# Performance work log

Hardware: AMD Instinct MI355X
Metric: run time of the kernel (lower is better)

Reference implementation:

```python
import jax, jax.numpy as jnp
import numpy as np

T, N, H = 512, 256, 256
HR, WC = 64, 128   # mdp rows (== n_actions), mdp cols
V = 64             # size of 'values' observation


def setup_inputs() -> dict:
    key = jax.random.key(0)
    ks = jax.random.split(key, 20)
    def p(i, shape):
        return (jax.random.normal(ks[i], shape, jnp.float32) / np.sqrt(shape[0])).astype(jnp.float32)
    z = lambda *s: jnp.zeros(s, jnp.float32)
    return dict(
        values=jax.random.normal(ks[0], (T, N, V), jnp.float32),
        mdp=jax.random.normal(ks[1], (N, HR, WC), jnp.float32),
        actions=jax.random.randint(ks[2], (T, N), 0, HR),
        a0=jax.random.randint(ks[3], (N,), 0, HR),
        h0=jax.random.normal(ks[4], (N, H), jnp.float32) * 0.1,
        emb_W=p(5, (WC, H)), emb_b=z(H),
        gfw_Wih=p(6, (H, 3 * H)), gfw_Whh=p(7, (H, 3 * H)), gfw_bih=z(3 * H), gfw_bhh=z(3 * H),
        gbw_Wih=p(8, (H, 3 * H)), gbw_Whh=p(9, (H, 3 * H)), gbw_bih=z(3 * H), gbw_bhh=z(3 * H),
        f0_W=p(10, (V + H, H)), f0_b=z(H),
        f1_W=p(11, (H, H)), f1_b=z(H),
        cell_Wih=p(12, (H, 3 * H)), cell_Whh=p(13, (H, 3 * H)), cell_bih=z(3 * H), cell_bhh=z(3 * H),
        critic_W=p(14, (H, 1)), critic_b=z(1),
        qg_W=p(15, (H, 2 * H)), qg_b=z(2 * H),
    )


def gru_step(x, h, Wih, Whh, bih, bhh):
    # torch GRU gate math: gates ordered (reset, update, new)
    gi = x @ Wih + bih
    gh = h @ Whh + bhh
    ir, iz, in_ = jnp.split(gi, 3, axis=-1)
    hr, hz, hn = jnp.split(gh, 3, axis=-1)
    r = jax.nn.sigmoid(ir + hr)
    z = jax.nn.sigmoid(iz + hz)
    n = jnp.tanh(in_ + r * hn)
    return (1.0 - z) * n + z * h


def run_gru(seq, Wih, Whh, bih, bhh):
    # seq: (S, N, H) -> outputs (S, N, H), zero initial state (torch default)
    h0g = jnp.zeros((seq.shape[1], Whh.shape[0]), seq.dtype)
    def step(h, x):
        hn = gru_step(x, h, Wih, Whh, bih, bhh)
        return hn, hn
    _, out = jax.lax.scan(step, h0g, seq)
    return out


def _forward(values, mdp, actions, a0, h0,
             emb_W, emb_b,
             gfw_Wih, gfw_Whh, gfw_bih, gfw_bhh,
             gbw_Wih, gbw_Whh, gbw_bih, gbw_bhh,
             f0_W, f0_b, f1_W, f1_b,
             cell_Wih, cell_Whh, cell_bih, cell_bhh,
             critic_W, critic_b, qg_W, qg_b):
    M = mdp @ emb_W + emb_b                      # (N, HR, H) line embeddings
    seq = jnp.swapaxes(M, 0, 1)                  # (HR, N, H) seq-first
    Kf = run_gru(seq, gfw_Wih, gfw_Whh, gfw_bih, gfw_bhh)
    Kb = run_gru(seq[::-1], gbw_Wih, gbw_Whh, gbw_bih, gbw_bhh)[::-1]
    K = jnp.swapaxes(jnp.concatenate([Kf, Kb], -1), 0, 1)   # (N, HR, 2H)

    a_prev = jnp.concatenate([a0[None], actions[:-1]], axis=0)  # A[t-1], t=0 wraps to hx.a
    batch = jnp.arange(M.shape[0])

    def step(h, xs):
        v_t, ap, ac = xs
        r = M[batch, ap]                         # one-hot(a_prev) @ M == row gather, (N, H)
        x = jnp.concatenate([v_t, r], axis=-1)
        x = jax.nn.relu(x @ f0_W + f0_b)
        x = jax.nn.relu(x @ f1_W + f1_b)
        h = gru_step(x, h, cell_Wih, cell_Whh, cell_bih, cell_bhh)
        k = h @ qg_W + qg_b                      # (N, 2H) query
        logits = jnp.einsum('nsd,nd->ns', K, k)  # (N, HR)
        probs = jax.nn.softmax(logits, axis=-1)
        v = h @ critic_W + critic_b              # (N, 1)
        return h, (ac.astype(jnp.float32)[:, None], v, h, probs)

    _, (a_out, v_out, h_out, p_out) = jax.lax.scan(step, h0, (values, a_prev, actions))
    # pack() order: RecurrentState fields 'a v h a_probs'
    hx = jnp.concatenate([a_out, v_out, h_out, p_out], axis=-1)  # (T, N, 2+H+HR)
    return hx


def reference(values, mdp, actions, a0, h0,
              emb_W, emb_b,
              gfw_Wih, gfw_Whh, gfw_bih, gfw_bhh,
              gbw_Wih, gbw_Whh, gbw_bih, gbw_bhh,
              f0_W, f0_b, f1_W, f1_b,
              cell_Wih, cell_Whh, cell_bih, cell_bhh,
              critic_W, critic_b, qg_W, qg_b):
    return _forward(values, mdp, actions, a0, h0,
                    emb_W, emb_b,
                    gfw_Wih, gfw_Whh, gfw_bih, gfw_bhh,
                    gbw_Wih, gbw_Whh, gbw_bih, gbw_bhh,
                    f0_W, f0_b, f1_W, f1_b,
                    cell_Wih, cell_Whh, cell_bih, cell_bhh,
                    critic_W, critic_b, qg_W, qg_b)
```

## Files before the change

kernel.cpp:

```cpp
#include <hip/hip_runtime.h>

#define TSTEPS 512
#define NBATCH 256
#define HID    256
#define TCHUNK 64
#define NCHUNK 8

typedef __attribute__((ext_vector_type(8))) short bf16x8;
typedef __attribute__((ext_vector_type(4))) float f32x4;

__device__ __forceinline__ unsigned short f2b(float x) {
    union { float f; unsigned int u; } c; c.f = x;
    unsigned int u = c.u;
    return (unsigned short)((u + 0x7fffu + ((u >> 16) & 1u)) >> 16);
}

__device__ __forceinline__ void gload_lds16(const float* g, float* l) {
    __builtin_amdgcn_global_load_lds(
        (const __attribute__((address_space(1))) unsigned int*)g,
        (__attribute__((address_space(3))) unsigned int*)l,
        16, 0, 0);
}

__device__ __forceinline__ int swzi(int row, int g) {
    return ((g ^ ((row >> 3) & 3)) << 3);
}

template<bool TRANS_B, int ACT>
__global__ __launch_bounds__(256) void gemm_f32(
    const float* __restrict__ A, long lda, long sA,
    const float* __restrict__ B, long ldb, long sB,
    const float* __restrict__ bias,
    float* __restrict__ C, long ldc, long sC,
    int M, int N, int K)
{
    __shared__ __align__(16) unsigned short As[64][32];
    __shared__ __align__(16) unsigned short Bs[64][32];
    const int z = blockIdx.z;
    A += (long)z * sA; B += (long)z * sB; C += (long)z * sC;
    const int n0 = blockIdx.x * 64, m0 = blockIdx.y * 64;
    const int tid  = threadIdx.x;
    const int lane = tid & 63, w = tid >> 6;
    const int wr = (w >> 1) * 32, wc = (w & 1) * 32;

    f32x4 acc[2][2];
#pragma unroll
    for (int i = 0; i < 2; i++)
#pragma unroll
        for (int j = 0; j < 2; j++) acc[i][j] = (f32x4){0.f, 0.f, 0.f, 0.f};

    for (int k0 = 0; k0 < K; k0 += 32) {
        {
            const int r = tid >> 2, ck = (tid & 3) << 3;
            const float* s = A + (long)(m0 + r) * lda + k0 + ck;
            float4 v0 = *(const float4*)s, v1 = *(const float4*)(s + 4);
            unsigned short* d = &As[r][swzi(r, ck >> 3)];
            d[0] = f2b(v0.x); d[1] = f2b(v0.y); d[2] = f2b(v0.z); d[3] = f2b(v0.w);
            d[4] = f2b(v1.x); d[5] = f2b(v1.y); d[6] = f2b(v1.z); d[7] = f2b(v1.w);
        }
        if (TRANS_B) {
            const int r = tid >> 2, ck = (tid & 3) << 3;
            const float* s = B + (long)(n0 + r) * ldb + k0 + ck;
            float4 v0 = *(const float4*)s, v1 = *(const float4*)(s + 4);
            unsigned short* d = &Bs[r][swzi(r, ck >> 3)];
            d[0] = f2b(v0.x); d[1] = f2b(v0.y); d[2] = f2b(v0.z); d[3] = f2b(v0.w);
            d[4] = f2b(v1.x); d[5] = f2b(v1.y); d[6] = f2b(v1.z); d[7] = f2b(v1.w);
        } else {
            const int kk = tid >> 3, cn = (tid & 7) << 3;
            const float* s = B + (long)(k0 + kk) * ldb + n0 + cn;
            float4 v0 = *(const float4*)s, v1 = *(const float4*)(s + 4);
            const int sc = swzi(cn, kk >> 3) + (kk & 7);
            Bs[cn + 0][sc] = f2b(v0.x); Bs[cn + 1][sc] = f2b(v0.y);
            Bs[cn + 2][sc] = f2b(v0.z); Bs[cn + 3][sc] = f2b(v0.w);
            Bs[cn + 4][sc] = f2b(v1.x); Bs[cn + 5][sc] = f2b(v1.y);
            Bs[cn + 6][sc] = f2b(v1.z); Bs[cn + 7][sc] = f2b(v1.w);
        }
        __syncthreads();
        const int l15 = lane & 15, q = lane >> 4;
        bf16x8 a0 = *(const bf16x8*)&As[wr +      l15][swzi(wr +      l15, q)];
        bf16x8 a1 = *(const bf16x8*)&As[wr + 16 + l15][swzi(wr + 16 + l15, q)];
        bf16x8 b0 = *(const bf16x8*)&Bs[wc +      l15][swzi(wc +      l15, q)];
        bf16x8 b1 = *(const bf16x8*)&Bs[wc + 16 + l15][swzi(wc + 16 + l15, q)];
        acc[0][0] = __builtin_amdgcn_mfma_f32_16x16x32_bf16(a0, b0, acc[0][0], 0, 0, 0);
        acc[0][1] = __builtin_amdgcn_mfma_f32_16x16x32_bf16(a0, b1, acc[0][1], 0, 0, 0);
        acc[1][0] = __builtin_amdgcn_mfma_f32_16x16x32_bf16(a1, b0, acc[1][0], 0, 0, 0);
        acc[1][1] = __builtin_amdgcn_mfma_f32_16x16x32_bf16(a1, b1, acc[1][1], 0, 0, 0);
        __syncthreads();
    }
    const int cq = lane >> 4, cc = lane & 15;
#pragma unroll
    for (int i = 0; i < 2; i++)
#pragma unroll
        for (int j = 0; j < 2; j++) {
#pragma unroll
            for (int rg = 0; rg < 4; rg++) {
                int row = m0 + wr + i * 16 + cq * 4 + rg;
                int col = n0 + wc + j * 16 + cc;
                float v = acc[i][j][rg];
                if (bias) v += bias[col];
                if (ACT == 1) v = v > 0.f ? v : 0.f;
                C[(long)row * ldc + col] = v;
            }
        }
}

__global__ void combine_bias(const float* a0, const float* b0,
                             const float* a1, const float* b1,
                             const float* a2, const float* b2,
                             float* o0, float* o1, float* o2)
{
    int i = blockIdx.x * 256 + threadIdx.x;
    o0[i] = a0[i] + b0[i];
    o1[i] = a1[i] + b1[i];
    o2[i] = a2[i] + b2[i];
}

__global__ void seq_major(const float* __restrict__ M, float* __restrict__ Mseq)
{
    int b = blockIdx.x;
    int s = b >> 8, n = b & 255;
    int t = threadIdx.x;
    Mseq[(long)b * 256 + t] = M[((long)n * 64 + s) * 256 + t];
}

__global__ __launch_bounds__(256) void pack_w(
    const float* __restrict__ Wf, const float* __restrict__ Wb, const float* __restrict__ Wc,
    unsigned short* __restrict__ Pf, unsigned short* __restrict__ Pb, unsigned short* __restrict__ Pc)
{
    int chunk = blockIdx.x * 256 + threadIdx.x;
    const float* W = (blockIdx.y == 0) ? Wf : ((blockIdx.y == 1) ? Wb : Wc);
    unsigned short* P = (blockIdx.y == 0) ? Pf : ((blockIdx.y == 1) ? Pb : Pc);
    int lane = chunk & 63;
    int kt   = (chunk >> 6) & 7;
    int f    = (chunk >> 9) % 6;
    int w    = chunk / 3072;
    int g = f >> 1, hh = f & 1;
    int c = lane & 15, q = lane >> 4;
    int col = g * 256 + w * 32 + hh * 16 + c;
    int k0  = kt * 32 + q * 8;
    unsigned int v[8];
#pragma unroll
    for (int j = 0; j < 8; j++) v[j] = f2b(W[(long)(k0 + j) * 768 + col]);
    uint4 o;
    o.x = v[0] | (v[1] << 16); o.y = v[2] | (v[3] << 16);
    o.z = v[4] | (v[5] << 16); o.w = v[6] | (v[7] << 16);
    *(uint4*)&P[(long)chunk * 8] = o;
}

__global__ void build_x(const float* __restrict__ values, const float* __restrict__ Mbuf,
                        const int* __restrict__ actions, const int* __restrict__ a0,
                        float* __restrict__ Xc, int t0)
{
    int m = blockIdx.x;
    int tl = m >> 8, n = m & 255;
    int t = t0 + tl;
    int c = threadIdx.x;
    float v;
    if (c < 64) {
        v = values[((long)t * 256 + n) * 64 + c];
    } else {
        int ap = (t == 0) ? a0[n] : actions[(long)(t - 1) * 256 + n];
        v = Mbuf[((long)n * 64 + ap) * 256 + (c - 64)];
    }
    Xc[(long)m * 320 + c] = v;
}

struct GemmRole {
    const float* A; const float* B; const float* bias; float* C;
    int K; long lda; long ldb; long ldc; int act; int nblocks; int ntn;
};

union FusedLds {
    struct { unsigned short hbuf[2][16][264]; float gibuf[2][16 * 772]; } s;
    struct { unsigned short As[64][32]; unsigned short Bs[128][32]; } g;
    struct { unsigned short As2[2][64][32]; unsigned short Bs2[2][64][32]; } l;
};

__device__ __forceinline__ void scan_role(FusedLds* L,
    const float* gi, const unsigned short* PK, const float* h_init,
    float* outp, float* h_state, int n0, int steps, int kgru, int d)
{
    auto& hbuf  = L->s.hbuf;
    auto& gibuf = L->s.gibuf;
    const int tid = threadIdx.x;
    const int w = tid >> 6, lane = tid & 63;
    const int q = lane >> 4, c = lane & 15, q8 = q << 3;
    const int wcol = w * 32;

    bf16x8 Bf[6][8];
#pragma unroll
    for (int f = 0; f < 6; f++)
#pragma unroll
        for (int kt = 0; kt < 8; kt++)
            Bf[f][kt] = *(const bf16x8*)&PK[(((long)(w * 6 + f) * 8 + kt) * 64 + lane) * 8];

    f32x4 hreg[2];
#pragma unroll
    for (int hh = 0; hh < 2; hh++)
#pragma unroll
        for (int rg = 0; rg < 4; rg++) {
            float v = 0.f;
            if (!kgru) v = h_init[(long)(n0 + q * 4 + rg) * 256 + wcol + hh * 16 + c];
            hreg[hh][rg] = v;
            hbuf[1][q * 4 + rg][wcol + hh * 16 + c] = f2b(v);
        }

    const int row0 = kgru ? (d ? 63 : 0) : 0;
    const long gstride = (kgru && d) ? -196608L : 196608L;
    const float* gsrc = gi + ((long)row0 * 256 + n0) * 768;
    float* optr[4];
    long ostride;
    if (kgru) {
        ostride = d ? -512L : 512L;
#pragma unroll
        for (int rg = 0; rg < 4; rg++)
            optr[rg] = outp + ((long)(n0 + q * 4 + rg) * 64 + row0) * 512 + d * 256 + wcol + c;
    } else {
        ostride = 65536L;
#pragma unroll
        for (int rg = 0; rg < 4; rg++)
            optr[rg] = outp + (long)(n0 + q * 4 + rg) * 256 + wcol + c;
    }

#pragma unroll
    for (int i = 0; i < 6; i++) {
        int idx = w * 6 + i;
        int r = idx / 3, ch = idx % 3;
        gload_lds16(gsrc + (long)r * 768 + ch * 256 + lane * 4,
                    &gibuf[0][r * 772 + ch * 256]);
    }
    __syncthreads();

    for (int s = 0; s < steps; s++) {
        const int cur = s & 1;
        if (s + 1 < steps) {
            const float* src = gsrc + gstride;
#pragma unroll
            for (int i = 0; i < 6; i++) {
                int idx = w * 6 + i;
                int r = idx / 3, ch = idx % 3;
                gload_lds16(src + (long)r * 768 + ch * 256 + lane * 4,
                            &gibuf[cur ^ 1][r * 772 + ch * 256]);
            }
        }
        gsrc += gstride;
        asm volatile("" ::: "memory");

        const unsigned short* hrd = &hbuf[cur ^ 1][0][0];
        const float* gp = &gibuf[cur][(q * 4) * 772 + wcol + c];
        unsigned short* hwr = &hbuf[cur][q * 4][wcol + c];

#pragma unroll
        for (int hh = 0; hh < 2; hh++) {
            f32x4 ar = (f32x4){0.f, 0.f, 0.f, 0.f};
            f32x4 az = (f32x4){0.f, 0.f, 0.f, 0.f};
            f32x4 an = (f32x4){0.f, 0.f, 0.f, 0.f};
#pragma unroll
            for (int kt = 0; kt < 8; kt++) {
                bf16x8 a = *(const bf16x8*)&hrd[c * 264 + kt * 32 + q8];
                ar = __builtin_amdgcn_mfma_f32_16x16x32_bf16(a, Bf[0 + hh][kt], ar, 0, 0, 0);
                az = __builtin_amdgcn_mfma_f32_16x16x32_bf16(a, Bf[2 + hh][kt], az, 0, 0, 0);
                an = __builtin_amdgcn_mfma_f32_16x16x32_bf16(a, Bf[4 + hh][kt], an, 0, 0, 0);
            }
#pragma unroll
            for (int rg = 0; rg < 4; rg++) {
                float gr = gp[rg * 772 +       hh * 16];
                float gz = gp[rg * 772 + 256 + hh * 16];
                float gn = gp[rg * 772 + 512 + hh * 16];
                float r  = __builtin_amdgcn_rcpf(1.f + __expf(-(gr + ar[rg])));
                float zg = __builtin_amdgcn_rcpf(1.f + __expf(-(gz + az[rg])));
                float nn = 1.f - 2.f * __builtin_amdgcn_rcpf(1.f + __expf(2.f * (gn + r * an[rg])));
                float hv = (1.f - zg) * nn + zg * hreg[hh][rg];
                hreg[hh][rg] = hv;
                hwr[rg * 264 + hh * 16] = f2b(hv);
                optr[rg][hh * 16] = hv;
            }
            asm volatile("" ::: "memory");
        }

#pragma unroll
        for (int rg = 0; rg < 4; rg++) optr[rg] += ostride;

        asm volatile("s_waitcnt vmcnt(8) lgkmcnt(0)" ::: "memory");
        __builtin_amdgcn_sched_barrier(0);
        __builtin_amdgcn_s_barrier();
        __builtin_amdgcn_sched_barrier(0);
    }

    if (!kgru) {
#pragma unroll
        for (int hh = 0; hh < 2; hh++)
#pragma unroll
            for (int rg = 0; rg < 4; rg++)
                h_state[(long)(n0 + q * 4 + rg) * 256 + wcol + hh * 16 + c] = hreg[hh][rg];
    }
}

__device__ __forceinline__ void gemm_role(FusedLds* L, const GemmRole& R, int rb)
{
    auto& As = L->g.As;
    auto& Bs = L->g.Bs;
    const int tid = threadIdx.x;
    const int lane = tid & 63, w = tid >> 6;
    const int mt = rb / R.ntn, nt = rb % R.ntn;
    const long m0 = (long)mt * 64, n0 = (long)nt * 128;
    const int wr = (w >> 2) * 32, wc = (w & 3) * 32;

    f32x4 acc[2][2];
#pragma unroll
    for (int i = 0; i < 2; i++)
#pragma unroll
        for (int j = 0; j < 2; j++) acc[i][j] = (f32x4){0.f, 0.f, 0.f, 0.f};

    for (int k0 = 0; k0 < R.K; k0 += 32) {
        {
            const int r = tid >> 3, ck = (tid & 7) << 2;
            const float* s = R.A + (m0 + r) * R.lda + k0 + ck;
            float4 v = *(const float4*)s;
            unsigned short* dp = &As[r][swzi(r, ck >> 3) + (ck & 7)];
            dp[0] = f2b(v.x); dp[1] = f2b(v.y); dp[2] = f2b(v.z); dp[3] = f2b(v.w);
        }
        {
            const int kk = tid >> 4, cn = (tid & 15) << 3;
            const float* s = R.B + (long)(k0 + kk) * R.ldb + n0 + cn;
            float4 v0 = *(const float4*)s, v1 = *(const float4*)(s + 4);
            const int sc = swzi(cn, kk >> 3) + (kk & 7);
            Bs[cn + 0][sc] = f2b(v0.x); Bs[cn + 1][sc] = f2b(v0.y);
            Bs[cn + 2][sc] = f2b(v0.z); Bs[cn + 3][sc] = f2b(v0.w);
            Bs[cn + 4][sc] = f2b(v1.x); Bs[cn + 5][sc] = f2b(v1.y);
            Bs[cn + 6][sc] = f2b(v1.z); Bs[cn + 7][sc] = f2b(v1.w);
        }
        __syncthreads();
        const int l15 = lane & 15, q = lane >> 4;
        bf16x8 a0 = *(const bf16x8*)&As[wr +      l15][swzi(wr +      l15, q)];
        bf16x8 a1 = *(const bf16x8*)&As[wr + 16 + l15][swzi(wr + 16 + l15, q)];
        bf16x8 b0 = *(const bf16x8*)&Bs[wc +      l15][swzi(wc +      l15, q)];
        bf16x8 b1 = *(const bf16x8*)&Bs[wc + 16 + l15][swzi(wc + 16 + l15, q)];
        acc[0][0] = __builtin_amdgcn_mfma_f32_16x16x32_bf16(a0, b0, acc[0][0], 0, 0, 0);
        acc[0][1] = __builtin_amdgcn_mfma_f32_16x16x32_bf16(a0, b1, acc[0][1], 0, 0, 0);
        acc[1][0] = __builtin_amdgcn_mfma_f32_16x16x32_bf16(a1, b0, acc[1][0], 0, 0, 0);
        acc[1][1] = __builtin_amdgcn_mfma_f32_16x16x32_bf16(a1, b1, acc[1][1], 0, 0, 0);
        __syncthreads();
    }
    const int cq = lane >> 4, cc = lane & 15;
#pragma unroll
    for (int i = 0; i < 2; i++)
#pragma unroll
        for (int j = 0; j < 2; j++) {
#pragma unroll
            for (int rg = 0; rg < 4; rg++) {
                long row = m0 + wr + i * 16 + cq * 4 + rg;
                long col = n0 + wc + j * 16 + cc;
                float v = acc[i][j][rg];
                if (R.bias) v += R.bias[col];
                if (R.act == 1) v = v > 0.f ? v : 0.f;
                R.C[row * R.ldc + col] = v;
            }
        }
}

__device__ __forceinline__ void logits_role(FusedLds* L, int rb,
    const float* Qs, const float* Kb, float* Lout)
{
    auto& As = L->l.As2;
    auto& Bs = L->l.Bs2;
    const int tid = threadIdx.x;
    const int half = tid >> 8, htid = tid & 255;
    const int z = rb * 2 + half;
    const float* A = Qs + (long)z * 512;
    const float* B = Kb + (long)z * 32768;
    float* C = Lout + (long)z * 64;
    const int lane = htid & 63, w4 = htid >> 6;
    const int wr = (w4 >> 1) * 32, wc = (w4 & 1) * 32;

    f32x4 acc[2][2];
#pragma unroll
    for (int i = 0; i < 2; i++)
#pragma unroll
        for (int j = 0; j < 2; j++) acc[i][j] = (f32x4){0.f, 0.f, 0.f, 0.f};

    for (int k0 = 0; k0 < 512; k0 += 32) {
        const int r = htid >> 2, ck = (htid & 3) << 3;
        {
            const float* s = A + (long)r * 131072 + k0 + ck;
            float4 v0 = *(const float4*)s, v1 = *(const float4*)(s + 4);
            unsigned short* d = &As[half][r][swzi(r, ck >> 3)];
            d[0] = f2b(v0.x); d[1] = f2b(v0.y); d[2] = f2b(v0.z); d[3] = f2b(v0.w);
            d[4] = f2b(v1.x); d[5] = f2b(v1.y); d[6] = f2b(v1.z); d[7] = f2b(v1.w);
        }
        {
            const float* s = B + (long)r * 512 + k0 + ck;
            float4 v0 = *(const float4*)s, v1 = *(const float4*)(s + 4);
            unsigned short* d = &Bs[half][r][swzi(r, ck >> 3)];
            d[0] = f2b(v0.x); d[1] = f2b(v0.y); d[2] = f2b(v0.z); d[3] = f2b(v0.w);
            d[4] = f2b(v1.x); d[5] = f2b(v1.y); d[6] = f2b(v1.z); d[7] = f2b(v1.w);
        }
        __syncthreads();
        const int l15 = lane & 15, q = lane >> 4;
        bf16x8 a0 = *(const bf16x8*)&As[half][wr +      l15][swzi(wr +      l15, q)];
        bf16x8 a1 = *(const bf16x8*)&As[half][wr + 16 + l15][swzi(wr + 16 + l15, q)];
        bf16x8 b0 = *(const bf16x8*)&Bs[half][wc +      l15][swzi(wc +      l15, q)];
        bf16x8 b1 = *(const bf16x8*)&Bs[half][wc + 16 + l15][swzi(wc + 16 + l15, q)];
        acc[0][0] = __builtin_amdgcn_mfma_f32_16x16x32_bf16(a0, b0, acc[0][0], 0, 0, 0);
        acc[0][1] = __builtin_amdgcn_mfma_f32_16x16x32_bf16(a0, b1, acc[0][1], 0, 0, 0);
        acc[1][0] = __builtin_amdgcn_mfma_f32_16x16x32_bf16(a1, b0, acc[1][0], 0, 0, 0);
        acc[1][1] = __builtin_amdgcn_mfma_f32_16x16x32_bf16(a1, b1, acc[1][1], 0, 0, 0);
        __syncthreads();
    }
    const int cq = lane >> 4, cc = lane & 15;
#pragma unroll
    for (int i = 0; i < 2; i++)
#pragma unroll
        for (int j = 0; j < 2; j++) {
#pragma unroll
            for (int rg = 0; rg < 4; rg++)
                C[(long)(wr + i * 16 + cq * 4 + rg) * 16384 + wc + j * 16 + cc] = acc[i][j][rg];
        }
}

__device__ __forceinline__ void epi_role(int rb,
    const float* Hall, const float* Lc, const int* actions,
    const float* critic_W, const float* critic_b, float* out, int t0)
{
    const int w = threadIdx.x >> 6, j = threadIdx.x & 63;
    const int m = rb * 8 + w;
    const int tl = m >> 8, n = m & 255;
    const int t = t0 + tl;
    long o = ((long)t * 256 + n) * 322;
    const float* h = Hall + (long)m * 256;
    float part = 0.f;
#pragma unroll
    for (int i = 0; i < 4; i++) {
        float hv = h[j + 64 * i];
        out[o + 2 + j + 64 * i] = hv;
        part += hv * critic_W[j + 64 * i];
    }
    for (int off = 32; off > 0; off >>= 1) part += __shfl_down(part, off);
    if (j == 0) {
        out[o]     = (float)actions[(long)t * 256 + n];
        out[o + 1] = part + critic_b[0];
    }
    float x = Lc[(long)m * 64 + j];
    float mx = x;
    for (int off = 32; off > 0; off >>= 1) mx = fmaxf(mx, __shfl_down(mx, off));
    mx = __shfl(mx, 0);
    float e = __expf(x - mx);
    float ssum = e;
    for (int off = 32; off > 0; off >>= 1) ssum += __shfl_down(ssum, off);
    ssum = __shfl(ssum, 0);
    out[o + 258 + j] = e / ssum;
}

__device__ __forceinline__ void bx_role(int rb,
    const float* values, const float* Mbuf, const int* actions, const int* a0,
    float* Xd, int t0)
{
    const int tid = threadIdx.x;
    if (tid >= 320) return;
    for (int rr = 0; rr < 128; rr++) {
        int m = rb * 128 + rr;
        int tl = m >> 8, n = m & 255;
        int t = t0 + tl;
        float v;
        if (tid < 64) {
            v = values[((long)t * 256 + n) * 64 + tid];
        } else {
            int ap = (t == 0) ? a0[n] : actions[(long)(t - 1) * 256 + n];
            v = Mbuf[((long)n * 64 + ap) * 256 + (tid - 64)];
        }
        Xd[(long)m * 320 + tid] = v;
    }
}

__global__ __launch_bounds__(512, 2) void fused_k(
    int sc_nblk, const float* sc_gi, const unsigned short* sc_PK, const float* sc_hinit,
    float* sc_out, float* sc_hstate,
    int kgru_nblk, const float* kg_gi0, const float* kg_gi1,
    const unsigned short* kg_PK0, const unsigned short* kg_PK1, float* kg_out,
    GemmRole g0, GemmRole g1, GemmRole g2, GemmRole g3, GemmRole g4, GemmRole g5,
    int lg_nblk, const float* lg_Q, const float* lg_K, float* lg_L,
    int ep_nblk, const float* ep_Hall, const float* ep_L, int ep_t0,
    int bx_nblk, const float* values, const float* Mbuf,
    const int* actions, const int* a0, float* bx_dst, int bx_t0,
    const float* critic_W, const float* critic_b, float* out)
{
    __shared__ __align__(16) FusedLds L;
    int b = blockIdx.x;
    if (b < sc_nblk) {
        scan_role(&L, sc_gi, sc_PK, sc_hinit, sc_out, sc_hstate, b * 16, TCHUNK, 0, 0);
        return;
    }
    b -= sc_nblk;
    if (b < kgru_nblk) {
        int d = b >> 4, n0 = (b & 15) * 16;
        scan_role(&L, d ? kg_gi1 : kg_gi0, d ? kg_PK1 : kg_PK0, nullptr,
                  kg_out, nullptr, n0, 64, 1, d);
        return;
    }
    b -= kgru_nblk;
    if (b < g0.nblocks) { gemm_role(&L, g0, b); return; }
    b -= g0.nblocks;
    if (b < g1.nblocks) { gemm_role(&L, g1, b); return; }
    b -= g1.nblocks;
    if (b < g2.nblocks) { gemm_role(&L, g2, b); return; }
    b -= g2.nblocks;
    if (b < g3.nblocks) { gemm_role(&L, g3, b); return; }
    b -= g3.nblocks;
    if (b < g4.nblocks) { gemm_role(&L, g4, b); return; }
    b -= g4.nblocks;
    if (b < g5.nblocks) { gemm_role(&L, g5, b); return; }
    b -= g5.nblocks;
    if (b < lg_nblk) { logits_role(&L, b, lg_Q, lg_K, lg_L); return; }
    b -= lg_nblk;
    if (b < ep_nblk) { epi_role(b, ep_Hall, ep_L, actions, critic_W, critic_b, out, ep_t0); return; }
    b -= ep_nblk;
    if (b < bx_nblk) bx_role(b, values, Mbuf, actions, a0, bx_dst, bx_t0);
}

__global__ __launch_bounds__(64) void epilogue_k(
    const float* __restrict__ Hallc, const float* __restrict__ Lc,
    const int* __restrict__ actions,
    const float* __restrict__ critic_W, const float* __restrict__ critic_b,
    float* __restrict__ out, int t0)
{
    int m = blockIdx.x;
    int tl = m >> 8, n = m & 255;
    int t = t0 + tl;
    int j = threadIdx.x;
    long o = ((long)t * 256 + n) * 322;
    const float* h = Hallc + (long)m * 256;
    float part = 0.f;
#pragma unroll
    for (int i = 0; i < 4; i++) {
        float hv = h[j + 64 * i];
        out[o + 2 + j + 64 * i] = hv;
        part += hv * critic_W[j + 64 * i];
    }
    for (int off = 32; off > 0; off >>= 1) part += __shfl_down(part, off);
    if (j == 0) {
        out[o]     = (float)actions[(long)t * 256 + n];
        out[o + 1] = part + critic_b[0];
    }
    float x = Lc[(long)m * 64 + j];
    float mx = x;
    for (int off = 32; off > 0; off >>= 1) mx = fmaxf(mx, __shfl_down(mx, off));
    mx = __shfl(mx, 0);
    float e = __expf(x - mx);
    float ssum = e;
    for (int off = 32; off > 0; off >>= 1) ssum += __shfl_down(ssum, off);
    ssum = __shfl(ssum, 0);
    out[o + 258 + j] = e / ssum;
}

extern "C" void kernel_launch(void* const* d_in, const int* in_sizes, int n_in,
                              void* d_out, int out_size, void* d_ws, size_t ws_size,
                              hipStream_t stream)
{
    const float* values   = (const float*)d_in[0];
    const float* mdp      = (const float*)d_in[1];
    const int*   actions  = (const int*)  d_in[2];
    const int*   a0       = (const int*)  d_in[3];
    const float* h0       = (const float*)d_in[4];
    const float* emb_W    = (const float*)d_in[5];
    const float* emb_b    = (const float*)d_in[6];
    const float* gfw_Wih  = (const float*)d_in[7];
    const float* gfw_Whh  = (const float*)d_in[8];
    const float* gfw_bih  = (const float*)d_in[9];
    const float* gfw_bhh  = (const float*)d_in[10];
    const float* gbw_Wih  = (const float*)d_in[11];
    const float* gbw_Whh  = (const float*)d_in[12];
    const float* gbw_bih  = (const float*)d_in[13];
    const float* gbw_bhh  = (const float*)d_in[14];
    const float* f0_W     = (const float*)d_in[15];
    const float* f0_b     = (const float*)d_in[16];
    const float* f1_W     = (const float*)d_in[17];
    const float* f1_b     = (const float*)d_in[18];
    const float* cell_Wih = (const float*)d_in[19];
    const float* cell_Whh = (const float*)d_in[20];
    const float* cell_bih = (const float*)d_in[21];
    const float* cell_bhh = (const float*)d_in[22];
    const float* critic_W = (const float*)d_in[23];
    const float* critic_b = (const float*)d_in[24];
    const float* qg_W     = (const float*)d_in[25];
    const float* qg_b     = (const float*)d_in[26];
    float* out = (float*)d_out;

    char* base = (char*)d_ws;
    size_t off = 0;
    auto alloc = [&](size_t nf) -> float* {
        float* p = (float*)(base + off);
        off += nf * sizeof(float);
        off = (off + 255) & ~(size_t)255;
        return p;
    };
    float* Mbuf   = alloc(16384ull * 256);
    float* Mseq   = alloc(16384ull * 256);
    float* gfA    = alloc(16384ull * 768);
    float* gbA    = alloc(16384ull * 768);
    float* Kbuf   = alloc(256ull * 64 * 512);
    float* PKf    = alloc(98304);
    float* PKb    = alloc(98304);
    float* PKc    = alloc(98304);
    float* hstate = alloc(256ull * 256);
    float* Xr[2]    = { alloc(16384ull * 320), alloc(16384ull * 320) };
    float* X0r[2]   = { alloc(16384ull * 256), alloc(16384ull * 256) };
    float* X1r[2]   = { alloc(16384ull * 256), alloc(16384ull * 256) };
    float* GIr[2]   = { alloc(16384ull * 768), alloc(16384ull * 768) };
    float* Hallr[4] = { alloc(16384ull * 256), alloc(16384ull * 256),
                        Mseq, alloc(16384ull * 256) };
    float* Qr[2]  = { alloc(16384ull * 512), gbA };
    float* Lr[2]  = { alloc(16384ull * 64), alloc(16384ull * 64) };
    float* bias_f = alloc(768);
    float* bias_b = alloc(768);
    float* bias_c = alloc(768);
    (void)ws_size; (void)in_sizes; (void)n_in; (void)out_size;

    dim3 blk(256);

    gemm_f32<false, 0><<<dim3(4, 256, 1), blk, 0, stream>>>(
        mdp, 128, 0, emb_W, 256, 0, emb_b, Mbuf, 256, 0, 16384, 256, 128);
    seq_major<<<dim3(16384), blk, 0, stream>>>(Mbuf, Mseq);
    pack_w<<<dim3(96, 3, 1), blk, 0, stream>>>(
        gfw_Whh, gbw_Whh, cell_Whh,
        (unsigned short*)PKf, (unsigned short*)PKb, (unsigned short*)PKc);
    combine_bias<<<dim3(3), blk, 0, stream>>>(gfw_bih, gfw_bhh, gbw_bih, gbw_bhh,
                                              cell_bih, cell_bhh, bias_f, bias_b, bias_c);

    build_x<<<dim3(16384), dim3(320), 0, stream>>>(values, Mbuf, actions, a0, Xr[0], 0);
    gemm_f32<false, 1><<<dim3(4, 256, 1), blk, 0, stream>>>(
        Xr[0], 320, 0, f0_W, 256, 0, f0_b, X0r[0], 256, 0, 16384, 256, 320);
    build_x<<<dim3(16384), dim3(320), 0, stream>>>(values, Mbuf, actions, a0, Xr[1], 64);
    gemm_f32<false, 1><<<dim3(4, 256, 1), blk, 0, stream>>>(
        Xr[1], 320, 0, f0_W, 256, 0, f0_b, X0r[1], 256, 0, 16384, 256, 320);
    gemm_f32<false, 1><<<dim3(4, 256, 1), blk, 0, stream>>>(
        X0r[0], 256, 0, f1_W, 256, 0, f1_b, X1r[0], 256, 0, 16384, 256, 256);
    build_x<<<dim3(16384), dim3(320), 0, stream>>>(values, Mbuf, actions, a0, Xr[0], 128);
    gemm_f32<false, 1><<<dim3(4, 256, 1), blk, 0, stream>>>(
        Xr[0], 320, 0, f0_W, 256, 0, f0_b, X0r[0], 256, 0, 16384, 256, 320);
    gemm_f32<false, 1><<<dim3(4, 256, 1), blk, 0, stream>>>(
        X0r[1], 256, 0, f1_W, 256, 0, f1_b, X1r[1], 256, 0, 16384, 256, 256);
    build_x<<<dim3(16384), dim3(320), 0, stream>>>(values, Mbuf, actions, a0, Xr[1], 192);
    gemm_f32<false, 0><<<dim3(12, 256, 1), blk, 0, stream>>>(
        X1r[0], 256, 0, cell_Wih, 768, 0, bias_c, GIr[0], 768, 0, 16384, 768, 256);

    for (int c = 0; c < NCHUNK; c++) {
        GemmRole g0{}, g1{}, g2{}, g3{}, g4{}, g5{};
        if (c <= 4) g0 = GemmRole{ Xr[(c + 1) & 1], f0_W, f0_b, X0r[(c + 1) & 1],
                                   320, 320, 256, 256, 1, 512, 2 };
        if (c <= 5) g1 = GemmRole{ X0r[c & 1], f1_W, f1_b, X1r[c & 1],
                                   256, 256, 256, 256, 1, 512, 2 };
        if (c <= 6) g2 = GemmRole{ X1r[(c + 1) & 1], cell_Wih, bias_c, GIr[(c + 1) & 1],
                                   256, 256, 768, 768, 0, 1536, 6 };
        if (c >= 1) g3 = GemmRole{ Hallr[(c - 1) & 3], qg_W, qg_b, Qr[(c - 1) & 1],
                                   256, 256, 512, 512, 0, 1024, 4 };
        if (c == 0) {
            g4 = GemmRole{ Mseq, gfw_Wih, bias_f, gfA, 256, 256, 768, 768, 0, 1536, 6 };
            g5 = GemmRole{ Mseq, gbw_Wih, bias_b, gbA, 256, 256, 768, 768, 0, 1536, 6 };
        }
        int kgn = (c == 1) ? 32 : 0;
        int lgn = (c >= 2) ? 128 : 0;
        int epn = (c >= 3) ? 2048 : 0;
        int bxn = (c <= 3) ? 128 : 0;
        int total = 16 + kgn + g0.nblocks + g1.nblocks + g2.nblocks + g3.nblocks
                    + g4.nblocks + g5.nblocks + lgn + epn + bxn;

        fused_k<<<dim3(total), dim3(512), 0, stream>>>(
            16, GIr[c & 1], (const unsigned short*)PKc, (c == 0) ? h0 : (const float*)hstate,
            Hallr[c & 3], hstate,
            kgn, gfA, gbA, (const unsigned short*)PKf, (const unsigned short*)PKb, Kbuf,
            g0, g1, g2, g3, g4, g5,
            lgn, Qr[(c - 2) & 1], Kbuf, Lr[(c - 2) & 1],
            epn, Hallr[(c - 3) & 3], Lr[(c - 3) & 1], (c - 3) * 64,
            bxn, values, Mbuf, actions, a0, Xr[c & 1], (c + 4) * 64,
            critic_W, critic_b, out);
    }

    {
        GemmRole gz{}, g3t = GemmRole{ Hallr[3], qg_W, qg_b, Qr[1],
                                       256, 256, 512, 512, 0, 1024, 4 };
        fused_k<<<dim3(1024 + 128 + 2048), dim3(512), 0, stream>>>(
            0, GIr[0], (const unsigned short*)PKc, hstate, Hallr[0], hstate,
            0, gfA, gbA, (const unsigned short*)PKf, (const unsigned short*)PKb, Kbuf,
            gz, gz, gz, g3t, gz, gz,
            128, Qr[0], Kbuf, Lr[0],
            2048, Hallr[1], Lr[1], 5 * 64,
            0, values, Mbuf, actions, a0, Xr[0], 0,
            critic_W, critic_b, out);
    }
    {
        GemmRole gz{};
        fused_k<<<dim3(128 + 2048), dim3(512), 0, stream>>>(
            0, GIr[0], (const unsigned short*)PKc, hstate, Hallr[0], hstate,
            0, gfA, gbA, (const unsigned short*)PKf, (const unsigned short*)PKb, Kbuf,
            gz, gz, gz, gz, gz, gz,
            128, Qr[1], Kbuf, Lr[1],
            2048, Hallr[2], Lr[0], 6 * 64,
            0, values, Mbuf, actions, a0, Xr[0], 0,
            critic_W, critic_b, out);
    }
    epilogue_k<<<dim3(16384), dim3(64), 0, stream>>>(
        Hallr[3], Lr[1], actions, critic_W, critic_b, out, 7 * 64);
}
```

Before: 2.202 ms.

## Store GRU input-gate precomputes in bf16 and raise fused kernel occupancy

The GEMMs that precompute GRU input projections (cell, forward and backward key GRUs) now write bf16 instead of fp32, through a new output-format flag. The scan role streams these bf16 gates into LDS with narrower async loads and widens them to fp32 before the gate math. This halves the per-step global traffic and LDS footprint on the sequential critical path. Separately, launch bounds for the fused kernel go from 2 to 4 blocks per CU, and Qr[1] gets its own buffer instead of aliasing gbA. The higher occupancy target squeezes the register budget. The scan role keeps its large register-resident weight fragments, so it risks spilling, and the bf16 gates lose some precision.

```diff
diff --git a/kernel.cpp b/kernel.cpp
--- a/kernel.cpp
+++ b/kernel.cpp
@@ -14,6 +14,10 @@
     unsigned int u = c.u;
     return (unsigned short)((u + 0x7fffu + ((u >> 16) & 1u)) >> 16);
 }
+__device__ __forceinline__ float b2f(unsigned short u) {
+    union { float f; unsigned int u; } c; c.u = ((unsigned int)u) << 16;
+    return c.f;
+}
 
 __device__ __forceinline__ void gload_lds16(const float* g, float* l) {
     __builtin_amdgcn_global_load_lds(
@@ -21,12 +25,24 @@
         (__attribute__((address_space(3))) unsigned int*)l,
         16, 0, 0);
 }
+__device__ __forceinline__ void gload_lds16u(const unsigned short* g, unsigned short* l) {
+    __builtin_amdgcn_global_load_lds(
+        (const __attribute__((address_space(1))) unsigned int*)g,
+        (__attribute__((address_space(3))) unsigned int*)l,
+        16, 0, 0);
+}
+__device__ __forceinline__ void gload_lds4u(const unsigned short* g, unsigned short* l) {
+    __builtin_amdgcn_global_load_lds(
+        (const __attribute__((address_space(1))) unsigned int*)g,
+        (__attribute__((address_space(3))) unsigned int*)l,
+        4, 0, 0);
+}
 
 __device__ __forceinline__ int swzi(int row, int g) {
     return ((g ^ ((row >> 3) & 3)) << 3);
 }
 
-template<bool TRANS_B, int ACT>
+template<bool TRANS_B, int ACT, int OBF>
 __global__ __launch_bounds__(256) void gemm_f32(
     const float* __restrict__ A, long lda, long sA,
     const float* __restrict__ B, long ldb, long sB,
@@ -99,7 +115,8 @@
                 float v = acc[i][j][rg];
                 if (bias) v += bias[col];
                 if (ACT == 1) v = v > 0.f ? v : 0.f;
-                C[(long)row * ldc + col] = v;
+                if (OBF) ((unsigned short*)C)[(long)row * ldc + col] = f2b(v);
+                else     C[(long)row * ldc + col] = v;
             }
         }
 }
@@ -167,17 +184,17 @@
 
 struct GemmRole {
     const float* A; const float* B; const float* bias; float* C;
-    int K; long lda; long ldb; long ldc; int act; int nblocks; int ntn;
+    int K; long lda; long ldb; long ldc; int act; int nblocks; int ntn; int obf;
 };
 
 union FusedLds {
-    struct { unsigned short hbuf[2][16][264]; float gibuf[2][16 * 772]; } s;
+    struct { unsigned short hbuf[2][16][264]; unsigned short gibuf[2][16 * 776]; } s;
     struct { unsigned short As[64][32]; unsigned short Bs[128][32]; } g;
     struct { unsigned short As2[2][64][32]; unsigned short Bs2[2][64][32]; } l;
 };
 
 __device__ __forceinline__ void scan_role(FusedLds* L,
-    const float* gi, const unsigned short* PK, const float* h_init,
+    const unsigned short* gi, const unsigned short* PK, const float* h_init,
     float* outp, float* h_state, int n0, int steps, int kgru, int d)
 {
     auto& hbuf  = L->s.hbuf;
@@ -207,7 +224,7 @@
 
     const int row0 = kgru ? (d ? 63 : 0) : 0;
     const long gstride = (kgru && d) ? -196608L : 196608L;
-    const float* gsrc = gi + ((long)row0 * 256 + n0) * 768;
+    const unsigned short* gsrc = gi + ((long)row0 * 256 + n0) * 768;
     float* optr[4];
     long ostride;
     if (kgru) {
@@ -225,29 +242,37 @@
 #pragma unroll
     for (int i = 0; i < 6; i++) {
         int idx = w * 6 + i;
-        int r = idx / 3, ch = idx % 3;
-        gload_lds16(gsrc + (long)r * 768 + ch * 256 + lane * 4,
-                    &gibuf[0][r * 772 + ch * 256]);
+        int r = idx / 3, kd = idx % 3;
+        if (kd == 0)
+            gload_lds16u(gsrc + (long)r * 768 + lane * 8, &gibuf[0][r * 776]);
+        else if (kd == 1)
+            gload_lds4u(gsrc + (long)r * 768 + 512 + lane * 2, &gibuf[0][r * 776 + 512]);
+        else
+            gload_lds4u(gsrc + (long)r * 768 + 640 + lane * 2, &gibuf[0][r * 776 + 640]);
     }
     __syncthreads();
 
     for (int s = 0; s < steps; s++) {
         const int cur = s & 1;
         if (s + 1 < steps) {
-            const float* src = gsrc + gstride;
+            const unsigned short* src = gsrc + gstride;
 #pragma unroll
             for (int i = 0; i < 6; i++) {
                 int idx = w * 6 + i;
-                int r = idx / 3, ch = idx % 3;
-                gload_lds16(src + (long)r * 768 + ch * 256 + lane * 4,
-                            &gibuf[cur ^ 1][r * 772 + ch * 256]);
+                int r = idx / 3, kd = idx % 3;
+                if (kd == 0)
+                    gload_lds16u(src + (long)r * 768 + lane * 8, &gibuf[cur ^ 1][r * 776]);
+                else if (kd == 1)
+                    gload_lds4u(src + (long)r * 768 + 512 + lane * 2, &gibuf[cur ^ 1][r * 776 + 512]);
+                else
+                    gload_lds4u(src + (long)r * 768 + 640 + lane * 2, &gibuf[cur ^ 1][r * 776 + 640]);
             }
         }
         gsrc += gstride;
         asm volatile("" ::: "memory");
 
         const unsigned short* hrd = &hbuf[cur ^ 1][0][0];
-        const float* gp = &gibuf[cur][(q * 4) * 772 + wcol + c];
+        const unsigned short* gp = &gibuf[cur][(q * 4) * 776 + wcol + c];
         unsigned short* hwr = &hbuf[cur][q * 4][wcol + c];
 
 #pragma unroll
@@ -264,9 +289,9 @@
             }
 #pragma unroll
             for (int rg = 0; rg < 4; rg++) {
-                float gr = gp[rg * 772 +       hh * 16];
-                float gz = gp[rg * 772 + 256 + hh * 16];
-                float gn = gp[rg * 772 + 512 + hh * 16];
+                float gr = b2f(gp[rg * 776 +       hh * 16]);
+                float gz = b2f(gp[rg * 776 + 256 + hh * 16]);
+                float gn = b2f(gp[rg * 776 + 512 + hh * 16]);
                 float r  = __builtin_amdgcn_rcpf(1.f + __expf(-(gr + ar[rg])));
                 float zg = __builtin_amdgcn_rcpf(1.f + __expf(-(gz + az[rg])));
                 float nn = 1.f - 2.f * __builtin_amdgcn_rcpf(1.f + __expf(2.f * (gn + r * an[rg])));
@@ -354,7 +379,8 @@
                 float v = acc[i][j][rg];
                 if (R.bias) v += R.bias[col];
                 if (R.act == 1) v = v > 0.f ? v : 0.f;
-                R.C[row * R.ldc + col] = v;
+                if (R.obf) ((unsigned short*)R.C)[row * R.ldc + col] = f2b(v);
+                else       R.C[row * R.ldc + col] = v;
             }
         }
 }
@@ -472,10 +498,10 @@
     }
 }
 
-__global__ __launch_bounds__(512, 2) void fused_k(
-    int sc_nblk, const float* sc_gi, const unsigned short* sc_PK, const float* sc_hinit,
-    float* sc_out, float* sc_hstate,
-    int kgru_nblk, const float* kg_gi0, const float* kg_gi1,
+__global__ __launch_bounds__(512, 4) void fused_k(
+    int sc_nblk, const unsigned short* sc_gi, const unsigned short* sc_PK,
+    const float* sc_hinit, float* sc_out, float* sc_hstate,
+    int kgru_nblk, const unsigned short* kg_gi0, const unsigned short* kg_gi1,
     const unsigned short* kg_PK0, const unsigned short* kg_PK1, float* kg_out,
     GemmRole g0, GemmRole g1, GemmRole g2, GemmRole g3, GemmRole g4, GemmRole g5,
     int lg_nblk, const float* lg_Q, const float* lg_K, float* lg_L,
@@ -595,8 +621,8 @@
     };
     float* Mbuf   = alloc(16384ull * 256);
     float* Mseq   = alloc(16384ull * 256);
-    float* gfA    = alloc(16384ull * 768);
-    float* gbA    = alloc(16384ull * 768);
+    unsigned short* gfA = (unsigned short*)alloc(16384ull * 384);
+    unsigned short* gbA = (unsigned short*)alloc(16384ull * 384);
     float* Kbuf   = alloc(256ull * 64 * 512);
     float* PKf    = alloc(98304);
     float* PKb    = alloc(98304);
@@ -605,10 +631,11 @@
     float* Xr[2]    = { alloc(16384ull * 320), alloc(16384ull * 320) };
     float* X0r[2]   = { alloc(16384ull * 256), alloc(16384ull * 256) };
     float* X1r[2]   = { alloc(16384ull * 256), alloc(16384ull * 256) };
-    float* GIr[2]   = { alloc(16384ull * 768), alloc(16384ull * 768) };
+    unsigned short* GIr[2] = { (unsigned short*)alloc(16384ull * 384),
+                               (unsigned short*)alloc(16384ull * 384) };
     float* Hallr[4] = { alloc(16384ull * 256), alloc(16384ull * 256),
                         Mseq, alloc(16384ull * 256) };
-    float* Qr[2]  = { alloc(16384ull * 512), gbA };
+    float* Qr[2]  = { alloc(16384ull * 512), alloc(16384ull * 512) };
     float* Lr[2]  = { alloc(16384ull * 64), alloc(16384ull * 64) };
     float* bias_f = alloc(768);
     float* bias_b = alloc(768);
@@ -617,7 +644,7 @@
 
     dim3 blk(256);
 
-    gemm_f32<false, 0><<<dim3(4, 256, 1), blk, 0, stream>>>(
+    gemm_f32<false, 0, 0><<<dim3(4, 256, 1), blk, 0, stream>>>(
         mdp, 128, 0, emb_W, 256, 0, emb_b, Mbuf, 256, 0, 16384, 256, 128);
     seq_major<<<dim3(16384), blk, 0, stream>>>(Mbuf, Mseq);
     pack_w<<<dim3(96, 3, 1), blk, 0, stream>>>(
@@ -627,35 +654,35 @@
                                               cell_bih, cell_bhh, bias_f, bias_b, bias_c);
 
     build_x<<<dim3(16384), dim3(320), 0, stream>>>(values, Mbuf, actions, a0, Xr[0], 0);
-    gemm_f32<false, 1><<<dim3(4, 256, 1), blk, 0, stream>>>(
+    gemm_f32<false, 1, 0><<<dim3(4, 256, 1), blk, 0, stream>>>(
         Xr[0], 320, 0, f0_W, 256, 0, f0_b, X0r[0], 256, 0, 16384, 256, 320);
     build_x<<<dim3(16384), dim3(320), 0, stream>>>(values, Mbuf, actions, a0, Xr[1], 64);
-    gemm_f32<false, 1><<<dim3(4, 256, 1), blk, 0, stream>>>(
+    gemm_f32<false, 1, 0><<<dim3(4, 256, 1), blk, 0, stream>>>(
         Xr[1], 320, 0, f0_W, 256, 0, f0_b, X0r[1], 256, 0, 16384, 256, 320);
-    gemm_f32<false, 1><<<dim3(4, 256, 1), blk, 0, stream>>>(
+    gemm_f32<false, 1, 0><<<dim3(4, 256, 1), blk, 0, stream>>>(
         X0r[0], 256, 0, f1_W, 256, 0, f1_b, X1r[0], 256, 0, 16384, 256, 256);
     build_x<<<dim3(16384), dim3(320), 0, stream>>>(values, Mbuf, actions, a0, Xr[0], 128);
-    gemm_f32<false, 1><<<dim3(4, 256, 1), blk, 0, stream>>>(
+    gemm_f32<false, 1, 0><<<dim3(4, 256, 1), blk, 0, stream>>>(
         Xr[0], 320, 0, f0_W, 256, 0, f0_b, X0r[0], 256, 0, 16384, 256, 320);
-    gemm_f32<false, 1><<<dim3(4, 256, 1), blk, 0, stream>>>(
+    gemm_f32<false, 1, 0><<<dim3(4, 256, 1), blk, 0, stream>>>(
         X0r[1], 256, 0, f1_W, 256, 0, f1_b, X1r[1], 256, 0, 16384, 256, 256);
     build_x<<<dim3(16384), dim3(320), 0, stream>>>(values, Mbuf, actions, a0, Xr[1], 192);
-    gemm_f32<false, 0><<<dim3(12, 256, 1), blk, 0, stream>>>(
-        X1r[0], 256, 0, cell_Wih, 768, 0, bias_c, GIr[0], 768, 0, 16384, 768, 256);
+    gemm_f32<false, 0, 1><<<dim3(12, 256, 1), blk, 0, stream>>>(
+        X1r[0], 256, 0, cell_Wih, 768, 0, bias_c, (float*)GIr[0], 768, 0, 16384, 768, 256);
 
     for (int c = 0; c < NCHUNK; c++) {
         GemmRole g0{}, g1{}, g2{}, g3{}, g4{}, g5{};
         if (c <= 4) g0 = GemmRole{ Xr[(c + 1) & 1], f0_W, f0_b, X0r[(c + 1) & 1],
-                                   320, 320, 256, 256, 1, 512, 2 };
+                                   320, 320, 256, 256, 1, 512, 2, 0 };
         if (c <= 5) g1 = GemmRole{ X0r[c & 1], f1_W, f1_b, X1r[c & 1],
-                                   256, 256, 256, 256, 1, 512, 2 };
-        if (c <= 6) g2 = GemmRole{ X1r[(c + 1) & 1], cell_Wih, bias_c, GIr[(c + 1) & 1],
-                                   256, 256, 768, 768, 0, 1536, 6 };
+                                   256, 256, 256, 256, 1, 512, 2, 0 };
+        if (c <= 6) g2 = GemmRole{ X1r[(c + 1) & 1], cell_Wih, bias_c, (float*)GIr[(c + 1) & 1],
+                                   256, 256, 768, 768, 0, 1536, 6, 1 };
         if (c >= 1) g3 = GemmRole{ Hallr[(c - 1) & 3], qg_W, qg_b, Qr[(c - 1) & 1],
-                                   256, 256, 512, 512, 0, 1024, 4 };
+                                   256, 256, 512, 512, 0, 1024, 4, 0 };
         if (c == 0) {
-            g4 = GemmRole{ Mseq, gfw_Wih, bias_f, gfA, 256, 256, 768, 768, 0, 1536, 6 };
-            g5 = GemmRole{ Mseq, gbw_Wih, bias_b, gbA, 256, 256, 768, 768, 0, 1536, 6 };
+            g4 = GemmRole{ Mseq, gfw_Wih, bias_f, (float*)gfA, 256, 256, 768, 768, 0, 1536, 6, 1 };
+            g5 = GemmRole{ Mseq, gbw_Wih, bias_b, (float*)gbA, 256, 256, 768, 768, 0, 1536, 6, 1 };
         }
         int kgn = (c == 1) ? 32 : 0;
         int lgn = (c >= 2) ? 128 : 0;
@@ -677,7 +704,7 @@
 
     {
         GemmRole gz{}, g3t = GemmRole{ Hallr[3], qg_W, qg_b, Qr[1],
-                                       256, 256, 512, 512, 0, 1024, 4 };
+                                       256, 256, 512, 512, 0, 1024, 4, 0 };
         fused_k<<<dim3(1024 + 128 + 2048), dim3(512), 0, stream>>>(
             0, GIr[0], (const unsigned short*)PKc, hstate, Hallr[0], hstate,
             0, gfA, gbA, (const unsigned short*)PKf, (const unsigned short*)PKb, Kbuf,
```

Result: slower. 5.951 ms (+170.3%).
